# Performance work log

Hardware: AMD Instinct MI355X
Metric: run time of the kernel (lower is better)

The kernel has to match this reference:

```python
import jax, jax.numpy as jnp
import numpy as np

N_VN = 8000
N_CN = 4000
DV = 3
DC = 6
BATCH = 1250
CODERATE = 0.5
NUM_ITER = 5
LLR_MAX = 20.0
EPS = 1e-12


def _build_graph():
    # regular (3,6) Tanner graph: 3 layers, each layer gives every VN one edge
    # and every CN two edges (n = 2m).
    rng = np.random.RandomState(0)
    vn = np.tile(np.arange(N_VN, dtype=np.int32), DV)
    cn_layers = []
    for _ in range(DV):
        cn_layers.append(rng.permutation(np.repeat(np.arange(N_CN, dtype=np.int32), 2)))
    cn = np.concatenate(cn_layers)
    return vn, cn


def setup_inputs() -> dict:
    key = jax.random.key(0)
    k1, = jax.random.split(key, 1)
    vn, cn = _build_graph()
    noise = jax.random.normal(k1, (BATCH, N_VN), dtype=jnp.float32)
    weights = jnp.ones((DV * N_VN,), dtype=jnp.float32)  # trainable edge weights, init 1
    return {
        "noise": noise,
        "weights": weights,
        "vn_idx": jnp.asarray(vn),
        "cn_idx": jnp.asarray(cn),
        "ebno_db": 4,
    }


def _bp_forward(noise, weights, vn_idx, cn_idx, ebno_db):
    B, n = noise.shape
    m = n // 2
    # ebnodb2no with 1 bit/symbol
    no = 1.0 / (10.0 ** (ebno_db / 10.0) * CODERATE)
    sigma2 = 4.0 / no
    # GaussianPriorSource: llr = log(p(x=1)/p(x=0)) for all-zero codeword
    llr = (-sigma2 / 2.0) + jnp.sqrt(sigma2) * noise  # [B, n]
    # decoder works internally with log(p0/p1); messages kept as [E, B]
    L = -llr.T  # [n, B]
    msg_vn = L[vn_idx]  # [E, B] initial VN->CN messages
    w = weights[:, None]

    loss = jnp.float32(0.0)
    c_hat = None
    for _ in range(NUM_ITER):
        # ---- check node update (boxplus, leave-one-out in log domain) ----
        mw = jnp.clip(msg_vn * w, -LLR_MAX, LLR_MAX)
        t = jnp.tanh(mw / 2.0)  # [E, B]
        log_t = jnp.log(jnp.maximum(jnp.abs(t), EPS))
        neg = (t < 0).astype(jnp.float32)
        sum_log = jax.ops.segment_sum(log_t, cn_idx, num_segments=m)  # [m, B]
        sum_neg = jax.ops.segment_sum(neg, cn_idx, num_segments=m)
        parity = jnp.mod(sum_neg[cn_idx] - neg, 2.0)
        sign = 1.0 - 2.0 * parity
        mag = jnp.exp(sum_log[cn_idx] - log_t)
        prod = jnp.clip(sign * mag, -1.0 + 1e-7, 1.0 - 1e-7)
        msg_cn = 2.0 * jnp.arctanh(prod)  # [E, B] CN->VN messages
        # ---- variable node update + marginalization ----
        x_tot = L + jax.ops.segment_sum(msg_cn, vn_idx, num_segments=n)  # [n, B]
        msg_vn = x_tot[vn_idx] - msg_cn
        c_hat = -x_tot.T  # back to log(p1/p0) convention, [B, n]
        # BCE(from_logits) with all-zero labels -> mean softplus(logits)
        loss = loss + jnp.mean(jax.nn.softplus(c_hat))
    loss = loss / NUM_ITER
    c = jnp.zeros((B, n), dtype=jnp.float32)
    return c, c_hat, llr, loss


def reference(noise, weights, vn_idx, cn_idx, ebno_db):
    return _bp_forward(noise, weights, vn_idx, cn_idx, ebno_db)
```

## Files before the change

kernel.cpp:

```cpp
#include <hip/hip_runtime.h>
#include <hip/hip_fp16.h>
#include <math.h>

constexpr int N_VN   = 8000;
constexpr int N_CN   = 4000;
constexpr int DV     = 3;
constexpr int DC     = 6;
constexpr int EDGES  = N_VN * DV;
constexpr int BATCH  = 1250;
constexpr int HBATCH = 625;
constexpr int NUM_ITER = 5;
constexpr float LLR_MAX = 20.0f;
constexpr float MSGMAX = 16.635532f;
constexpr float FFLOOR = 2e-12f;
constexpr float QSCALE = 32767.0f / 20.0f;
constexpr float QINV   = 20.0f / 32767.0f;
constexpr float LOG2E  = 1.44269504f;
constexpr float LN2    = 0.69314718f;
constexpr float C3     = QSCALE * LN2;
constexpr float QMSGMAX = MSGMAX * QSCALE;

constexpr int MTPB  = 1024;
constexpr int VREM  = N_VN - 7 * MTPB;
constexpr int CREM  = N_CN - 3 * MTPB;

__device__ __forceinline__ unsigned pack_sex2(float mv0, float mv1, float w) {
    float mw0 = fminf(fmaxf(mv0 * w, -LLR_MAX), LLR_MAX);
    float mw1 = fminf(fmaxf(mv1 * w, -LLR_MAX), LLR_MAX);
    float e0 = exp2f(-fabsf(mw0) * LOG2E);
    float e1 = exp2f(-fabsf(mw1) * LOG2E);
    float s0 = __uint_as_float(__float_as_uint(e0) | (__float_as_uint(mw0) & 0x80000000u));
    float s1 = __uint_as_float(__float_as_uint(e1) | (__float_as_uint(mw1) & 0x80000000u));
    auto hp = __builtin_amdgcn_cvt_pkrtz(s0, s1);
    unsigned u;
    __builtin_memcpy(&u, &hp, 4);
    return u;
}

__device__ __forceinline__ float half_bits_to_f32(unsigned short hbits) {
    __half h = __ushort_as_half(hbits);
    return __half2float(h);
}

__global__ __launch_bounds__(256) void build_graph_k(const int* __restrict__ cn_idx,
                                                     int* __restrict__ cnt,
                                                     int* __restrict__ epos) {
    int e = blockIdx.x * 256 + threadIdx.x;
    if (e >= EDGES) return;
    int c = cn_idx[e];
    int slot = atomicAdd(&cnt[c], 1);
    epos[e] = slot * N_CN + c;
}

__global__ __launch_bounds__(256) void pack_k(const int* __restrict__ epos,
                                              const float* __restrict__ weights,
                                              ushort4* __restrict__ vp4,
                                              float4* __restrict__ wf4) {
    int v = blockIdx.x * 256 + threadIdx.x;
    if (v >= N_VN) return;
    vp4[v] = make_ushort4((unsigned short)epos[v],
                          (unsigned short)epos[v + N_VN],
                          (unsigned short)epos[v + 2 * N_VN], 0);
    wf4[v] = make_float4(weights[v], weights[v + N_VN], weights[v + 2 * N_VN], 0.0f);
}

__global__ __launch_bounds__(MTPB) void bp_mega_k(const float* __restrict__ noise,
                                                  const ushort4* __restrict__ vp4,
                                                  const float4* __restrict__ wf4,
                                                  const int* __restrict__ ebno,
                                                  float* __restrict__ llr_out,
                                                  float* __restrict__ chat_out,
                                                  float* __restrict__ c_out,
                                                  float* __restrict__ loss_part) {
    __shared__ unsigned eSu[N_CN * DC];
    __shared__ float hs[2];
    __shared__ float red[MTPB / 64];

    const int b   = blockIdx.x;
    const int tid = threadIdx.x;

    if (tid == 0) {
        double sig2 = 2.0 * pow(10.0, (double)ebno[0] * 0.1);
        hs[0] = (float)(sig2 * 0.5);
        hs[1] = (float)sqrt(sig2);
    }
    __syncthreads();
    const float h = hs[0], s = hs[1];

    const float* nrow0 = noise    + (size_t)b * N_VN;
    const float* nrow1 = noise    + (size_t)(b + HBATCH) * N_VN;
    float*       lrow0 = llr_out  + (size_t)b * N_VN;
    float*       lrow1 = llr_out  + (size_t)(b + HBATCH) * N_VN;
    float*       crow0 = chat_out + (size_t)b * N_VN;
    float*       crow1 = chat_out + (size_t)(b + HBATCH) * N_VN;
    float*       zrow0 = c_out    + (size_t)b * N_VN;
    float*       zrow1 = c_out    + (size_t)(b + HBATCH) * N_VN;

    float L0[8], L1[8];
    int   pp[8][DV];
    float wr_[8][DV];
    #pragma unroll
    for (int r = 0; r < 8; ++r) {
        int v = tid + r * MTPB;
        if (r < 7 || tid < VREM) {
            float n0 = nrow0[v], n1 = nrow1[v];
            float llr0 = fmaf(s, n0, -h), llr1 = fmaf(s, n1, -h);
            lrow0[v] = llr0; lrow1[v] = llr1;
            zrow0[v] = 0.0f; zrow1[v] = 0.0f;
            L0[r] = -llr0; L1[r] = -llr1;
            ushort4 p4 = vp4[v];
            float4  w4 = wf4[v];
            pp[r][0] = p4.x; pp[r][1] = p4.y; pp[r][2] = p4.z;
            wr_[r][0] = w4.x; wr_[r][1] = w4.y; wr_[r][2] = w4.z;
            #pragma unroll
            for (int l = 0; l < DV; ++l)
                eSu[pp[r][l]] = pack_sex2(L0[r], L1[r], wr_[r][l]);
        }
    }

    float spMax = 0.0f, spLog = 0.0f;
    #pragma unroll 1
    for (int it = 0; it < NUM_ITER; ++it) {
        __syncthreads();
        #pragma unroll
        for (int k = 0; k < 4; ++k) {
            int c = tid + k * MTPB;
            if (k < 3 || tid < CREM) {
                unsigned d[DC];
                float f0[DC], f1[DC];
                float n0 = 1.0f, de0 = 1.0f, n1 = 1.0f, de1 = 1.0f;
                unsigned sx = 0u;
                #pragma unroll
                for (int j = 0; j < DC; ++j) {
                    d[j] = eSu[c + j * N_CN];
                    sx ^= d[j];
                    float s0 = half_bits_to_f32((unsigned short)d[j]);
                    float s1 = half_bits_to_f32((unsigned short)(d[j] >> 16));
                    float F0 = fmaxf(1.0f - fabsf(s0), FFLOOR);
                    float F1 = fmaxf(1.0f - fabsf(s1), FFLOOR);
                    f0[j] = F0; f1[j] = F1;
                    n0 *= F0; de0 *= (2.0f - F0);
                    n1 *= F1; de1 *= (2.0f - F1);
                }
                float T0 = __fdividef(n0, de0);
                float T1 = __fdividef(n1, de1);
                #pragma unroll
                for (int j = 0; j < DC; ++j) {
                    float g0 = T0 * (2.0f - f0[j]);
                    float g1 = T1 * (2.0f - f1[j]);
                    float r0 = __fdividef(f0[j] + g0, f0[j] - g0);
                    float r1 = __fdividef(f1[j] + g1, f1[j] - g1);
                    float q0 = fminf(__log2f(r0) * C3, QMSGMAX);
                    float q1 = fminf(__log2f(r1) * C3, QMSGMAX);
                    unsigned sp = sx ^ d[j];
                    float m0 = __uint_as_float(__float_as_uint(q0) ^ ((sp & 0x8000u) << 16));
                    float m1 = __uint_as_float(__float_as_uint(q1) ^ (sp & 0x80000000u));
                    int i0 = __float2int_rn(m0);
                    int i1 = __float2int_rn(m1);
                    eSu[c + j * N_CN] = ((unsigned)i0 & 0xffffu) | ((unsigned)i1 << 16);
                }
            }
        }
        __syncthreads();
        const bool wr = (it != NUM_ITER - 1);
        #pragma unroll
        for (int r = 0; r < 8; ++r) {
            int v = tid + r * MTPB;
            if (r < 7 || tid < VREM) {
                unsigned da = eSu[pp[r][0]];
                unsigned db = eSu[pp[r][1]];
                unsigned dc = eSu[pp[r][2]];
                int a0 = (int)(short)da, a1 = (int)da >> 16;
                int b0 = (int)(short)db, b1 = (int)db >> 16;
                int c0 = (int)(short)dc, c1 = (int)dc >> 16;
                float xt0 = fmaf((float)(a0 + b0 + c0), QINV, L0[r]);
                float xt1 = fmaf((float)(a1 + b1 + c1), QINV, L1[r]);
                if (wr) {
                    float ma0 = fmaf((float)a0, -QINV, xt0);
                    float ma1 = fmaf((float)a1, -QINV, xt1);
                    float mb0 = fmaf((float)b0, -QINV, xt0);
                    float mb1 = fmaf((float)b1, -QINV, xt1);
                    float mc0 = fmaf((float)c0, -QINV, xt0);
                    float mc1 = fmaf((float)c1, -QINV, xt1);
                    eSu[pp[r][0]] = pack_sex2(ma0, ma1, wr_[r][0]);
                    eSu[pp[r][1]] = pack_sex2(mb0, mb1, wr_[r][1]);
                    eSu[pp[r][2]] = pack_sex2(mc0, mc1, wr_[r][2]);
                } else {
                    crow0[v] = -xt0;
                    crow1[v] = -xt1;
                }
                spMax += fmaxf(-xt0, 0.0f) + fmaxf(-xt1, 0.0f);
                spLog += __log2f(1.0f + exp2f(-fabsf(xt0) * LOG2E));
                spLog += __log2f(1.0f + exp2f(-fabsf(xt1) * LOG2E));
            }
        }
    }
    float lossacc = fmaf(LN2, spLog, spMax);

    #pragma unroll
    for (int off = 32; off > 0; off >>= 1)
        lossacc += __shfl_down(lossacc, off, 64);
    int lane = tid & 63, wid = tid >> 6;
    if (lane == 0) red[wid] = lossacc;
    __syncthreads();
    if (tid == 0) {
        float ssum = 0.0f;
        #pragma unroll
        for (int i = 0; i < MTPB / 64; ++i) ssum += red[i];
        loss_part[b] = ssum;
    }
}

__global__ __launch_bounds__(256) void loss_final_k(const float* __restrict__ lp,
                                                    float* __restrict__ out_loss) {
    double s = 0.0;
    for (int i = threadIdx.x; i < HBATCH; i += 256) s += (double)lp[i];
    #pragma unroll
    for (int off = 32; off > 0; off >>= 1)
        s += __shfl_down(s, off, 64);
    __shared__ double red[4];
    int lane = threadIdx.x & 63, wid = threadIdx.x >> 6;
    if (lane == 0) red[wid] = s;
    __syncthreads();
    if (threadIdx.x == 0)
        out_loss[0] = (float)((red[0] + red[1] + red[2] + red[3]) /
                              ((double)NUM_ITER * (double)BATCH * (double)N_VN));
}

extern "C" void kernel_launch(void* const* d_in, const int* in_sizes, int n_in,
                              void* d_out, int out_size, void* d_ws, size_t ws_size,
                              hipStream_t stream) {
    const float* noise   = (const float*)d_in[0];
    const float* weights = (const float*)d_in[1];
    const int* cn_idx    = (const int*)d_in[3];
    const int* ebno      = (const int*)d_in[4];

    float* out      = (float*)d_out;
    float* out_c    = out;
    float* out_chat = out + 10000000;
    float* out_llr  = out + 20000000;
    float* out_loss = out + 30000000;

    char* ws = (char*)d_ws;
    int*     epos      = (int*)(ws);
    int*     cn_cnt    = (int*)(ws + 96000);
    ushort4* vp4       = (ushort4*)(ws + 112000);
    float4*  wf4       = (float4*)(ws + 176000);
    float*   loss_part = (float*)(ws + 304000);

    (void)hipMemsetAsync(cn_cnt, 0, N_CN * sizeof(int), stream);
    build_graph_k<<<dim3((EDGES + 255) / 256), dim3(256), 0, stream>>>(cn_idx, cn_cnt, epos);
    pack_k<<<dim3((N_VN + 255) / 256), dim3(256), 0, stream>>>(epos, weights, vp4, wf4);

    bp_mega_k<<<dim3(HBATCH), dim3(MTPB), 0, stream>>>(noise, vp4, wf4, ebno,
                                                       out_llr, out_chat, out_c, loss_part);

    loss_final_k<<<dim3(1), dim3(256), 0, stream>>>(loss_part, out_loss);
}
```

Baseline: 424.3 us.

## Process five batch rows per block and build graph in-kernel

The graph-build and pack kernels are removed; each block now builds the CN slot map in shared memory with shared atomics. Grid shrinks from 625 to 250 blocks, each decoding two fp16-packed row pairs plus one row in fp32 shared memory, which fits 250 blocks on the CUs in a single wave. This trades the tail and extra launches for redundant per-block graph construction and serial processing of five rows per block.

```diff
diff --git a/kernel.cpp b/kernel.cpp
--- a/kernel.cpp
+++ b/kernel.cpp
@@ -8,8 +8,8 @@
 constexpr int DC     = 6;
 constexpr int EDGES  = N_VN * DV;
 constexpr int BATCH  = 1250;
-constexpr int HBATCH = 625;
 constexpr int NUM_ITER = 5;
+constexpr int NBLK   = 250;
 constexpr float LLR_MAX = 20.0f;
 constexpr float MSGMAX = 16.635532f;
 constexpr float FFLOOR = 2e-12f;
@@ -38,163 +38,249 @@
 }
 
 __device__ __forceinline__ float half_bits_to_f32(unsigned short hbits) {
-    __half h = __ushort_as_half(hbits);
-    return __half2float(h);
-}
-
-__global__ __launch_bounds__(256) void build_graph_k(const int* __restrict__ cn_idx,
-                                                     int* __restrict__ cnt,
-                                                     int* __restrict__ epos) {
-    int e = blockIdx.x * 256 + threadIdx.x;
-    if (e >= EDGES) return;
-    int c = cn_idx[e];
-    int slot = atomicAdd(&cnt[c], 1);
-    epos[e] = slot * N_CN + c;
-}
-
-__global__ __launch_bounds__(256) void pack_k(const int* __restrict__ epos,
-                                              const float* __restrict__ weights,
-                                              ushort4* __restrict__ vp4,
-                                              float4* __restrict__ wf4) {
-    int v = blockIdx.x * 256 + threadIdx.x;
-    if (v >= N_VN) return;
-    vp4[v] = make_ushort4((unsigned short)epos[v],
-                          (unsigned short)epos[v + N_VN],
-                          (unsigned short)epos[v + 2 * N_VN], 0);
-    wf4[v] = make_float4(weights[v], weights[v + N_VN], weights[v + 2 * N_VN], 0.0f);
+    return __half2float(__ushort_as_half(hbits));
+}
+
+__device__ __forceinline__ float pack_ex(float mv, float w) {
+    float mw = fminf(fmaxf(mv * w, -LLR_MAX), LLR_MAX);
+    float ex = exp2f(-fabsf(mw) * LOG2E);
+    return __uint_as_float(__float_as_uint(ex) | (__float_as_uint(mw) & 0x80000000u));
 }
 
 __global__ __launch_bounds__(MTPB) void bp_mega_k(const float* __restrict__ noise,
-                                                  const ushort4* __restrict__ vp4,
-                                                  const float4* __restrict__ wf4,
+                                                  const float* __restrict__ weights,
+                                                  const int* __restrict__ cn_idx,
                                                   const int* __restrict__ ebno,
                                                   float* __restrict__ llr_out,
                                                   float* __restrict__ chat_out,
                                                   float* __restrict__ c_out,
                                                   float* __restrict__ loss_part) {
-    __shared__ unsigned eSu[N_CN * DC];
+    __shared__ unsigned eSu[EDGES];
     __shared__ float hs[2];
     __shared__ float red[MTPB / 64];
 
-    const int b   = blockIdx.x;
-    const int tid = threadIdx.x;
+    const int tid  = threadIdx.x;
+    const int base = blockIdx.x * 5;
 
     if (tid == 0) {
         double sig2 = 2.0 * pow(10.0, (double)ebno[0] * 0.1);
         hs[0] = (float)(sig2 * 0.5);
         hs[1] = (float)sqrt(sig2);
     }
+
+    int*            cnt   = (int*)eSu;
+    unsigned short* eposS = (unsigned short*)(eSu + 4000);
+    #pragma unroll
+    for (int k = 0; k < 4; ++k) {
+        int i = tid + k * MTPB;
+        if (k < 3 || tid < CREM) cnt[i] = 0;
+    }
     __syncthreads();
-    const float h = hs[0], s = hs[1];
-
-    const float* nrow0 = noise    + (size_t)b * N_VN;
-    const float* nrow1 = noise    + (size_t)(b + HBATCH) * N_VN;
-    float*       lrow0 = llr_out  + (size_t)b * N_VN;
-    float*       lrow1 = llr_out  + (size_t)(b + HBATCH) * N_VN;
-    float*       crow0 = chat_out + (size_t)b * N_VN;
-    float*       crow1 = chat_out + (size_t)(b + HBATCH) * N_VN;
-    float*       zrow0 = c_out    + (size_t)b * N_VN;
-    float*       zrow1 = c_out    + (size_t)(b + HBATCH) * N_VN;
-
-    float L0[8], L1[8];
+    for (int e = tid; e < EDGES; e += MTPB) {
+        int c = cn_idx[e];
+        int slot = atomicAdd(&cnt[c], 1);
+        eposS[e] = (unsigned short)(slot * N_CN + c);
+    }
+    __syncthreads();
     int   pp[8][DV];
-    float wr_[8][DV];
+    float wt[8][DV];
     #pragma unroll
     for (int r = 0; r < 8; ++r) {
         int v = tid + r * MTPB;
         if (r < 7 || tid < VREM) {
-            float n0 = nrow0[v], n1 = nrow1[v];
-            float llr0 = fmaf(s, n0, -h), llr1 = fmaf(s, n1, -h);
-            lrow0[v] = llr0; lrow1[v] = llr1;
-            zrow0[v] = 0.0f; zrow1[v] = 0.0f;
-            L0[r] = -llr0; L1[r] = -llr1;
-            ushort4 p4 = vp4[v];
-            float4  w4 = wf4[v];
-            pp[r][0] = p4.x; pp[r][1] = p4.y; pp[r][2] = p4.z;
-            wr_[r][0] = w4.x; wr_[r][1] = w4.y; wr_[r][2] = w4.z;
-            #pragma unroll
-            for (int l = 0; l < DV; ++l)
-                eSu[pp[r][l]] = pack_sex2(L0[r], L1[r], wr_[r][l]);
-        }
-    }
+            #pragma unroll
+            for (int l = 0; l < DV; ++l) {
+                pp[r][l] = eposS[v + l * N_VN];
+                wt[r][l] = weights[v + l * N_VN];
+            }
+        }
+    }
+    const float h = hs[0], s = hs[1];
 
     float spMax = 0.0f, spLog = 0.0f;
-    #pragma unroll 1
-    for (int it = 0; it < NUM_ITER; ++it) {
+
+    auto run_pair = [&](int b0i, int b1i) {
+        const float* nrow0 = noise    + (size_t)b0i * N_VN;
+        const float* nrow1 = noise    + (size_t)b1i * N_VN;
+        float*       lrow0 = llr_out  + (size_t)b0i * N_VN;
+        float*       lrow1 = llr_out  + (size_t)b1i * N_VN;
+        float*       crow0 = chat_out + (size_t)b0i * N_VN;
+        float*       crow1 = chat_out + (size_t)b1i * N_VN;
+        float*       zrow0 = c_out    + (size_t)b0i * N_VN;
+        float*       zrow1 = c_out    + (size_t)b1i * N_VN;
+        float L0[8], L1[8];
         __syncthreads();
-        #pragma unroll
-        for (int k = 0; k < 4; ++k) {
-            int c = tid + k * MTPB;
-            if (k < 3 || tid < CREM) {
-                unsigned d[DC];
-                float f0[DC], f1[DC];
-                float n0 = 1.0f, de0 = 1.0f, n1 = 1.0f, de1 = 1.0f;
-                unsigned sx = 0u;
-                #pragma unroll
-                for (int j = 0; j < DC; ++j) {
-                    d[j] = eSu[c + j * N_CN];
-                    sx ^= d[j];
-                    float s0 = half_bits_to_f32((unsigned short)d[j]);
-                    float s1 = half_bits_to_f32((unsigned short)(d[j] >> 16));
-                    float F0 = fmaxf(1.0f - fabsf(s0), FFLOOR);
-                    float F1 = fmaxf(1.0f - fabsf(s1), FFLOOR);
-                    f0[j] = F0; f1[j] = F1;
-                    n0 *= F0; de0 *= (2.0f - F0);
-                    n1 *= F1; de1 *= (2.0f - F1);
-                }
-                float T0 = __fdividef(n0, de0);
-                float T1 = __fdividef(n1, de1);
-                #pragma unroll
-                for (int j = 0; j < DC; ++j) {
-                    float g0 = T0 * (2.0f - f0[j]);
-                    float g1 = T1 * (2.0f - f1[j]);
-                    float r0 = __fdividef(f0[j] + g0, f0[j] - g0);
-                    float r1 = __fdividef(f1[j] + g1, f1[j] - g1);
-                    float q0 = fminf(__log2f(r0) * C3, QMSGMAX);
-                    float q1 = fminf(__log2f(r1) * C3, QMSGMAX);
-                    unsigned sp = sx ^ d[j];
-                    float m0 = __uint_as_float(__float_as_uint(q0) ^ ((sp & 0x8000u) << 16));
-                    float m1 = __uint_as_float(__float_as_uint(q1) ^ (sp & 0x80000000u));
-                    int i0 = __float2int_rn(m0);
-                    int i1 = __float2int_rn(m1);
-                    eSu[c + j * N_CN] = ((unsigned)i0 & 0xffffu) | ((unsigned)i1 << 16);
-                }
-            }
-        }
-        __syncthreads();
-        const bool wr = (it != NUM_ITER - 1);
         #pragma unroll
         for (int r = 0; r < 8; ++r) {
             int v = tid + r * MTPB;
             if (r < 7 || tid < VREM) {
-                unsigned da = eSu[pp[r][0]];
-                unsigned db = eSu[pp[r][1]];
-                unsigned dc = eSu[pp[r][2]];
-                int a0 = (int)(short)da, a1 = (int)da >> 16;
-                int b0 = (int)(short)db, b1 = (int)db >> 16;
-                int c0 = (int)(short)dc, c1 = (int)dc >> 16;
-                float xt0 = fmaf((float)(a0 + b0 + c0), QINV, L0[r]);
-                float xt1 = fmaf((float)(a1 + b1 + c1), QINV, L1[r]);
-                if (wr) {
-                    float ma0 = fmaf((float)a0, -QINV, xt0);
-                    float ma1 = fmaf((float)a1, -QINV, xt1);
-                    float mb0 = fmaf((float)b0, -QINV, xt0);
-                    float mb1 = fmaf((float)b1, -QINV, xt1);
-                    float mc0 = fmaf((float)c0, -QINV, xt0);
-                    float mc1 = fmaf((float)c1, -QINV, xt1);
-                    eSu[pp[r][0]] = pack_sex2(ma0, ma1, wr_[r][0]);
-                    eSu[pp[r][1]] = pack_sex2(mb0, mb1, wr_[r][1]);
-                    eSu[pp[r][2]] = pack_sex2(mc0, mc1, wr_[r][2]);
-                } else {
-                    crow0[v] = -xt0;
-                    crow1[v] = -xt1;
+                float n0 = nrow0[v], n1 = nrow1[v];
+                float llr0 = fmaf(s, n0, -h), llr1 = fmaf(s, n1, -h);
+                lrow0[v] = llr0; lrow1[v] = llr1;
+                zrow0[v] = 0.0f; zrow1[v] = 0.0f;
+                L0[r] = -llr0; L1[r] = -llr1;
+                #pragma unroll
+                for (int l = 0; l < DV; ++l)
+                    eSu[pp[r][l]] = pack_sex2(L0[r], L1[r], wt[r][l]);
+            }
+        }
+        #pragma unroll 1
+        for (int it = 0; it < NUM_ITER; ++it) {
+            __syncthreads();
+            #pragma unroll
+            for (int k = 0; k < 4; ++k) {
+                int c = tid + k * MTPB;
+                if (k < 3 || tid < CREM) {
+                    unsigned d[DC];
+                    float f0[DC], f1[DC];
+                    float n0 = 1.0f, de0 = 1.0f, n1 = 1.0f, de1 = 1.0f;
+                    unsigned sx = 0u;
+                    #pragma unroll
+                    for (int j = 0; j < DC; ++j) {
+                        d[j] = eSu[c + j * N_CN];
+                        sx ^= d[j];
+                        float s0 = half_bits_to_f32((unsigned short)d[j]);
+                        float s1 = half_bits_to_f32((unsigned short)(d[j] >> 16));
+                        float F0 = fmaxf(1.0f - fabsf(s0), FFLOOR);
+                        float F1 = fmaxf(1.0f - fabsf(s1), FFLOOR);
+                        f0[j] = F0; f1[j] = F1;
+                        n0 *= F0; de0 *= (2.0f - F0);
+                        n1 *= F1; de1 *= (2.0f - F1);
+                    }
+                    float T0 = __fdividef(n0, de0);
+                    float T1 = __fdividef(n1, de1);
+                    #pragma unroll
+                    for (int j = 0; j < DC; ++j) {
+                        float g0 = T0 * (2.0f - f0[j]);
+                        float g1 = T1 * (2.0f - f1[j]);
+                        float r0 = __fdividef(f0[j] + g0, f0[j] - g0);
+                        float r1 = __fdividef(f1[j] + g1, f1[j] - g1);
+                        float q0 = fminf(__log2f(r0) * C3, QMSGMAX);
+                        float q1 = fminf(__log2f(r1) * C3, QMSGMAX);
+                        unsigned sp = sx ^ d[j];
+                        float m0 = __uint_as_float(__float_as_uint(q0) ^ ((sp & 0x8000u) << 16));
+                        float m1 = __uint_as_float(__float_as_uint(q1) ^ (sp & 0x80000000u));
+                        int i0 = __float2int_rn(m0);
+                        int i1 = __float2int_rn(m1);
+                        eSu[c + j * N_CN] = ((unsigned)i0 & 0xffffu) | ((unsigned)i1 << 16);
+                    }
                 }
-                spMax += fmaxf(-xt0, 0.0f) + fmaxf(-xt1, 0.0f);
-                spLog += __log2f(1.0f + exp2f(-fabsf(xt0) * LOG2E));
-                spLog += __log2f(1.0f + exp2f(-fabsf(xt1) * LOG2E));
-            }
-        }
-    }
+            }
+            __syncthreads();
+            const bool wr = (it != NUM_ITER - 1);
+            #pragma unroll
+            for (int r = 0; r < 8; ++r) {
+                int v = tid + r * MTPB;
+                if (r < 7 || tid < VREM) {
+                    unsigned da = eSu[pp[r][0]];
+                    unsigned db = eSu[pp[r][1]];
+                    unsigned dc = eSu[pp[r][2]];
+                    int a0 = (int)(short)da, a1 = (int)da >> 16;
+                    int b0 = (int)(short)db, b1 = (int)db >> 16;
+                    int c0 = (int)(short)dc, c1 = (int)dc >> 16;
+                    float xt0 = fmaf((float)(a0 + b0 + c0), QINV, L0[r]);
+                    float xt1 = fmaf((float)(a1 + b1 + c1), QINV, L1[r]);
+                    if (wr) {
+                        float ma0 = fmaf((float)a0, -QINV, xt0);
+                        float ma1 = fmaf((float)a1, -QINV, xt1);
+                        float mb0 = fmaf((float)b0, -QINV, xt0);
+                        float mb1 = fmaf((float)b1, -QINV, xt1);
+                        float mc0 = fmaf((float)c0, -QINV, xt0);
+                        float mc1 = fmaf((float)c1, -QINV, xt1);
+                        eSu[pp[r][0]] = pack_sex2(ma0, ma1, wt[r][0]);
+                        eSu[pp[r][1]] = pack_sex2(mb0, mb1, wt[r][1]);
+                        eSu[pp[r][2]] = pack_sex2(mc0, mc1, wt[r][2]);
+                    } else {
+                        crow0[v] = -xt0;
+                        crow1[v] = -xt1;
+                    }
+                    spMax += fmaxf(-xt0, 0.0f) + fmaxf(-xt1, 0.0f);
+                    spLog += __log2f(1.0f + exp2f(-fabsf(xt0) * LOG2E));
+                    spLog += __log2f(1.0f + exp2f(-fabsf(xt1) * LOG2E));
+                }
+            }
+        }
+    };
+
+    auto run_single = [&](int b0i) {
+        float* eSf = (float*)eSu;
+        const float* nrow = noise    + (size_t)b0i * N_VN;
+        float*       lrow = llr_out  + (size_t)b0i * N_VN;
+        float*       crow = chat_out + (size_t)b0i * N_VN;
+        float*       zrow = c_out    + (size_t)b0i * N_VN;
+        float Lr[8];
+        __syncthreads();
+        #pragma unroll
+        for (int r = 0; r < 8; ++r) {
+            int v = tid + r * MTPB;
+            if (r < 7 || tid < VREM) {
+                float nv  = nrow[v];
+                float llr = fmaf(s, nv, -h);
+                lrow[v] = llr;
+                zrow[v] = 0.0f;
+                Lr[r] = -llr;
+                #pragma unroll
+                for (int l = 0; l < DV; ++l)
+                    eSf[pp[r][l]] = pack_ex(Lr[r], wt[r][l]);
+            }
+        }
+        #pragma unroll 1
+        for (int it = 0; it < NUM_ITER; ++it) {
+            __syncthreads();
+            #pragma unroll
+            for (int k = 0; k < 4; ++k) {
+                int c = tid + k * MTPB;
+                if (k < 3 || tid < CREM) {
+                    float se[DC], f[DC];
+                    float num = 1.0f, den = 1.0f;
+                    unsigned sx = 0u;
+                    #pragma unroll
+                    for (int j = 0; j < DC; ++j) {
+                        se[j] = eSf[c + j * N_CN];
+                        float F = fmaxf(1.0f - fabsf(se[j]), FFLOOR);
+                        f[j] = F;
+                        num *= F; den *= (2.0f - F);
+                        sx ^= __float_as_uint(se[j]);
+                    }
+                    float T = __fdividef(num, den);
+                    #pragma unroll
+                    for (int j = 0; j < DC; ++j) {
+                        float g  = T * (2.0f - f[j]);
+                        float rr = __fdividef(f[j] + g, f[j] - g);
+                        float ma = fminf(__log2f(rr) * LN2, MSGMAX);
+                        unsigned sg = (sx ^ __float_as_uint(se[j])) & 0x80000000u;
+                        eSf[c + j * N_CN] = __uint_as_float(__float_as_uint(ma) ^ sg);
+                    }
+                }
+            }
+            __syncthreads();
+            const bool wr = (it != NUM_ITER - 1);
+            #pragma unroll
+            for (int r = 0; r < 8; ++r) {
+                int v = tid + r * MTPB;
+                if (r < 7 || tid < VREM) {
+                    float m0 = eSf[pp[r][0]];
+                    float m1 = eSf[pp[r][1]];
+                    float m2 = eSf[pp[r][2]];
+                    float xt = Lr[r] + m0 + m1 + m2;
+                    if (wr) {
+                        eSf[pp[r][0]] = pack_ex(xt - m0, wt[r][0]);
+                        eSf[pp[r][1]] = pack_ex(xt - m1, wt[r][1]);
+                        eSf[pp[r][2]] = pack_ex(xt - m2, wt[r][2]);
+                    } else {
+                        crow[v] = -xt;
+                    }
+                    spMax += fmaxf(-xt, 0.0f);
+                    spLog += __log2f(1.0f + exp2f(-fabsf(xt) * LOG2E));
+                }
+            }
+        }
+    };
+
+    run_pair(base, base + 1);
+    run_pair(base + 2, base + 3);
+    run_single(base + 4);
+
     float lossacc = fmaf(LN2, spLog, spMax);
 
     #pragma unroll
@@ -207,14 +293,14 @@
         float ssum = 0.0f;
         #pragma unroll
         for (int i = 0; i < MTPB / 64; ++i) ssum += red[i];
-        loss_part[b] = ssum;
+        loss_part[blockIdx.x] = ssum;
     }
 }
 
 __global__ __launch_bounds__(256) void loss_final_k(const float* __restrict__ lp,
                                                     float* __restrict__ out_loss) {
     double s = 0.0;
-    for (int i = threadIdx.x; i < HBATCH; i += 256) s += (double)lp[i];
+    for (int i = threadIdx.x; i < NBLK; i += 256) s += (double)lp[i];
     #pragma unroll
     for (int off = 32; off > 0; off >>= 1)
         s += __shfl_down(s, off, 64);
@@ -241,19 +327,10 @@
     float* out_llr  = out + 20000000;
     float* out_loss = out + 30000000;
 
-    char* ws = (char*)d_ws;
-    int*     epos      = (int*)(ws);
-    int*     cn_cnt    = (int*)(ws + 96000);
-    ushort4* vp4       = (ushort4*)(ws + 112000);
-    float4*  wf4       = (float4*)(ws + 176000);
-    float*   loss_part = (float*)(ws + 304000);
-
-    (void)hipMemsetAsync(cn_cnt, 0, N_CN * sizeof(int), stream);
-    build_graph_k<<<dim3((EDGES + 255) / 256), dim3(256), 0, stream>>>(cn_idx, cn_cnt, epos);
-    pack_k<<<dim3((N_VN + 255) / 256), dim3(256), 0, stream>>>(epos, weights, vp4, wf4);
-
-    bp_mega_k<<<dim3(HBATCH), dim3(MTPB), 0, stream>>>(noise, vp4, wf4, ebno,
-                                                       out_llr, out_chat, out_c, loss_part);
+    float* loss_part = (float*)d_ws;
+
+    bp_mega_k<<<dim3(NBLK), dim3(MTPB), 0, stream>>>(noise, weights, cn_idx, ebno,
+                                                     out_llr, out_chat, out_c, loss_part);
 
     loss_final_k<<<dim3(1), dim3(256), 0, stream>>>(loss_part, out_loss);
 }
```

After: 389.4 us. 1.09x faster.
